# Performance work log

Measured on AMD Instinct MI355X. Metric: run time of the kernel, lower is better.

Reference implementation:

```python
import jax, jax.numpy as jnp
import numpy as np

N_NODES = 50000
N_EDGES = 800000
NH, FOUT, FIN = 4, 32, 128
LEAKY_SLOPE = 0.2


def setup_inputs() -> dict:
    key = jax.random.key(0)
    k1, k2, k3, k4, k5 = jax.random.split(key, 5)
    x = jax.random.normal(k1, (N_NODES, FIN), dtype=jnp.float32)
    edge_index = jax.random.randint(k2, (2, N_EDGES), 0, N_NODES, dtype=jnp.int64)
    W = jax.random.normal(k3, (FIN, NH * FOUT), dtype=jnp.float32) * (1.0 / np.sqrt(FIN))
    a_src = jax.random.normal(k4, (NH, FOUT), dtype=jnp.float32)
    a_trg = jax.random.normal(k5, (NH, FOUT), dtype=jnp.float32)
    bias = jnp.zeros((NH * FOUT,), dtype=jnp.float32)
    return {"x": x, "edge_index": edge_index, "W": W, "a_src": a_src, "a_trg": a_trg, "bias": bias}


def reference(x, edge_index, W, a_src, a_trg, bias):
    N = x.shape[0]
    # Step 1: linear projection (dropout omitted: eval mode)
    proj = (x @ W).reshape(N, NH, FOUT)              # (N, NH, FOUT)
    # Per-head attention scores for each node as source / target
    s_src = jnp.einsum('nhf,hf->nh', proj, a_src)    # (N, NH)
    s_trg = jnp.einsum('nhf,hf->nh', proj, a_trg)    # (N, NH)
    # Step 2: lift to edges (gather) and score
    src, trg = edge_index[0], edge_index[1]
    e = jax.nn.leaky_relu(s_src[src] + s_trg[trg], LEAKY_SLOPE)   # (E, NH)
    # Step 3: neighborhood-aware softmax (global max shift, as in GAT imp3)
    exp_e = jnp.exp(e - e.max())                      # (E, NH)
    denom = jax.ops.segment_sum(exp_e, trg, num_segments=N)       # (N, NH)
    att = exp_e / (denom[trg] + 1e-16)                # (E, NH)
    # Step 4: weight lifted source features and scatter-aggregate to targets
    weighted = proj[src] * att[:, :, None]            # (E, NH, FOUT)
    out = jax.ops.segment_sum(weighted, trg, num_segments=N)      # (N, NH, FOUT)
    # Step 5: skip connection (FIN == NH*FOUT -> direct add), concat heads, bias, ELU
    out = out + x.reshape(N, NH, FOUT)
    out = out.reshape(N, NH * FOUT) + bias
    return jax.nn.elu(out)
```

## Files before the change

### kernel.cpp

```cpp
#include <hip/hip_runtime.h>
#include <stdint.h>

typedef __attribute__((ext_vector_type(8))) short short8;
typedef __attribute__((ext_vector_type(4))) float floatx4;

__device__ inline float bf2f(unsigned short b) {
    unsigned u = ((unsigned)b) << 16;
    return __builtin_bit_cast(float, u);
}
__device__ inline unsigned short f2bf(float f) {
    unsigned u = __builtin_bit_cast(unsigned, f);
    unsigned r = (u + 0x7fffu + ((u >> 16) & 1u)) >> 16;
    return (unsigned short)r;
}
__device__ inline float ldf(const void* p, int i, int f32) {
    return f32 ? ((const float*)p)[i] : bf2f(((const unsigned short*)p)[i]);
}
__device__ inline int lde(const int* ei, int idx, int is64) {
    return is64 ? ei[2 * idx] : ei[idx];
}

__global__ __launch_bounds__(256) void k_pre(
    const void* __restrict__ x, const int* __restrict__ ei,
    const void* __restrict__ W, int* __restrict__ flags,
    unsigned short* __restrict__ WhT, unsigned short* __restrict__ WlT,
    int* __restrict__ counts, int N)
{
    int b = blockIdx.x;
    int t = threadIdx.x;
    if (b == 0) {
        __shared__ int h1, h2;
        if (t == 0) { h1 = 0; h2 = 0; }
        __syncthreads();
        const unsigned short* xs = (const unsigned short*)x;
        int c1 = 0;
        for (int i = t * 2; i < 65536; i += 512)
            if ((xs[i] & 0x7f80u) == 0x7f80u) c1++;
        int c2 = 0;
        for (int i = t * 2 + 1; i < 8192; i += 512)
            if (ei[i] != 0) c2++;
        atomicAdd(&h1, c1);
        atomicAdd(&h2, c2);
        __syncthreads();
        if (t == 0) { flags[0] = (h1 >= 8); flags[1] = (h2 < 8); }
    } else if (b <= 64) {
        __shared__ int wcnt;
        if (t == 0) wcnt = 0;
        __syncthreads();
        const unsigned short* wsamp = (const unsigned short*)W;
        int c = 0;
        for (int i = t * 2; i < 16384; i += 512)
            if ((wsamp[i] & 0x7f80u) == 0x7f80u) c++;
        atomicAdd(&wcnt, c);
        __syncthreads();
        int f32 = (wcnt >= 8);
        int idx = (b - 1) * 256 + t;
        int n = idx >> 7, k = idx & 127;
        float v = ldf(W, k * 128 + n, f32);
        unsigned short h = f2bf(v);
        WhT[idx] = h;
        WlT[idx] = f2bf(v - bf2f(h));
    } else {
        int idx = (b - 65) * 256 + t;
        if (idx <= N) counts[idx] = 0;
    }
}

__global__ __launch_bounds__(256) void k1_gemm(
    const void* __restrict__ x, const unsigned short* __restrict__ WhT,
    const unsigned short* __restrict__ WlT, const void* __restrict__ a_src,
    const void* __restrict__ a_trg, const int* __restrict__ flags,
    unsigned short* __restrict__ projb, float* __restrict__ ssrc,
    float* __restrict__ strg, int N)
{
    __shared__ __align__(16) unsigned short WT[128 * 136];
    int t = threadIdx.x;
    int f32 = flags[0];
    for (int i = t; i < 2048; i += 256) {
        int row = i >> 4, ch = (i & 15) * 8;
        *(short8*)&WT[row * 136 + ch] = *(const short8*)&WhT[row * 128 + ch];
    }
    __syncthreads();
    int wave = t >> 6, lane = t & 63;
    int col = lane & 15, quad = lane >> 4;
    int row0 = blockIdx.x * 64 + wave * 16;
    int m = row0 + col;
    if (m >= N) m = N - 1;
    short8 ah[4], al[4];
    if (f32) {
        const float* xf = (const float*)x + (size_t)m * 128 + quad * 8;
#pragma unroll
        for (int kb = 0; kb < 4; kb++) {
            float4 v0 = *(const float4*)(xf + kb * 32);
            float4 v1 = *(const float4*)(xf + kb * 32 + 4);
            float vv[8] = {v0.x, v0.y, v0.z, v0.w, v1.x, v1.y, v1.z, v1.w};
#pragma unroll
            for (int j = 0; j < 8; j++) {
                unsigned short h = f2bf(vv[j]);
                ah[kb][j] = (short)h;
                al[kb][j] = (short)f2bf(vv[j] - bf2f(h));
            }
        }
    } else {
        const unsigned short* xb = (const unsigned short*)x + (size_t)m * 128 + quad * 8;
#pragma unroll
        for (int kb = 0; kb < 4; kb++)
            ah[kb] = *(const short8*)(xb + kb * 32);
    }
    floatx4 acc[8];
#pragma unroll
    for (int c = 0; c < 8; c++) acc[c] = (floatx4){0.f, 0.f, 0.f, 0.f};
#pragma unroll
    for (int c = 0; c < 8; c++) {
        const short8* bp = (const short8*)(&WT[(c * 16 + col) * 136 + quad * 8]);
        short8 b0 = bp[0], b1 = bp[4], b2 = bp[8], b3 = bp[12];
        acc[c] = __builtin_amdgcn_mfma_f32_16x16x32_bf16(ah[0], b0, acc[c], 0, 0, 0);
        acc[c] = __builtin_amdgcn_mfma_f32_16x16x32_bf16(ah[1], b1, acc[c], 0, 0, 0);
        acc[c] = __builtin_amdgcn_mfma_f32_16x16x32_bf16(ah[2], b2, acc[c], 0, 0, 0);
        acc[c] = __builtin_amdgcn_mfma_f32_16x16x32_bf16(ah[3], b3, acc[c], 0, 0, 0);
        if (f32) {
            acc[c] = __builtin_amdgcn_mfma_f32_16x16x32_bf16(al[0], b0, acc[c], 0, 0, 0);
            acc[c] = __builtin_amdgcn_mfma_f32_16x16x32_bf16(al[1], b1, acc[c], 0, 0, 0);
            acc[c] = __builtin_amdgcn_mfma_f32_16x16x32_bf16(al[2], b2, acc[c], 0, 0, 0);
            acc[c] = __builtin_amdgcn_mfma_f32_16x16x32_bf16(al[3], b3, acc[c], 0, 0, 0);
        }
    }
    if (f32) {
        __syncthreads();
        for (int i = t; i < 2048; i += 256) {
            int row = i >> 4, ch = (i & 15) * 8;
            *(short8*)&WT[row * 136 + ch] = *(const short8*)&WlT[row * 128 + ch];
        }
        __syncthreads();
#pragma unroll
        for (int c = 0; c < 8; c++) {
            const short8* bp = (const short8*)(&WT[(c * 16 + col) * 136 + quad * 8]);
            acc[c] = __builtin_amdgcn_mfma_f32_16x16x32_bf16(ah[0], bp[0], acc[c], 0, 0, 0);
            acc[c] = __builtin_amdgcn_mfma_f32_16x16x32_bf16(ah[1], bp[4], acc[c], 0, 0, 0);
            acc[c] = __builtin_amdgcn_mfma_f32_16x16x32_bf16(ah[2], bp[8], acc[c], 0, 0, 0);
            acc[c] = __builtin_amdgcn_mfma_f32_16x16x32_bf16(ah[3], bp[12], acc[c], 0, 0, 0);
        }
    }
#pragma unroll
    for (int r = 0; r < 4; r++) {
        int row = row0 + quad * 4 + r;
        if (row < N) {
#pragma unroll
            for (int c = 0; c < 8; c++)
                projb[(size_t)row * 128 + c * 16 + col] = f2bf(acc[c][r]);
        }
    }
    float asv[8], atv[8];
#pragma unroll
    for (int c = 0; c < 8; c++) {
        int j = c * 16 + col;
        asv[c] = ldf(a_src, j, f32);
        atv[c] = ldf(a_trg, j, f32);
    }
#pragma unroll
    for (int r = 0; r < 4; r++) {
        int row = row0 + quad * 4 + r;
        float ps[4] = {0.f, 0.f, 0.f, 0.f}, pt[4] = {0.f, 0.f, 0.f, 0.f};
#pragma unroll
        for (int c = 0; c < 8; c++) {
            int h = c >> 1;
            ps[h] += acc[c][r] * asv[c];
            pt[h] += acc[c][r] * atv[c];
        }
#pragma unroll
        for (int k = 1; k < 16; k <<= 1) {
#pragma unroll
            for (int h = 0; h < 4; h++) {
                ps[h] += __shfl_xor(ps[h], k, 16);
                pt[h] += __shfl_xor(pt[h], k, 16);
            }
        }
        if (col == 0 && row < N) {
#pragma unroll
            for (int h = 0; h < 4; h++) {
                ssrc[(size_t)row * 4 + h] = ps[h];
                strg[(size_t)row * 4 + h] = pt[h];
            }
        }
    }
}

__device__ inline void edge_scores(const float* ssrc, const float* strg,
                                   int src, int trg, float* v) {
    float4 a = *(const float4*)(ssrc + (size_t)src * 4);
    float4 b = *(const float4*)(strg + (size_t)trg * 4);
    v[0] = a.x + b.x; v[1] = a.y + b.y; v[2] = a.z + b.z; v[3] = a.w + b.w;
#pragma unroll
    for (int h = 0; h < 4; h++) v[h] = v[h] > 0.f ? v[h] : 0.2f * v[h];
}

__global__ __launch_bounds__(256) void kE_count_max(
    const int* __restrict__ ei, const float* __restrict__ ssrc,
    const float* __restrict__ strg, const int* __restrict__ flags,
    int* __restrict__ counts, uint4* __restrict__ epackI,
    float4* __restrict__ epackV, float* __restrict__ blockmax, int E, int N)
{
    int e64 = flags[1];
    int e = blockIdx.x * 256 + threadIdx.x;
    float m = -3.0e38f;
    if (e < E) {
        int src = min(max(lde(ei, e, e64), 0), N - 1);
        int trg = min(max(lde(ei, E + e, e64), 0), N - 1);
        int rank = atomicAdd(&counts[trg], 1);
        float v[4];
        edge_scores(ssrc, strg, src, trg, v);
        m = fmaxf(fmaxf(v[0], v[1]), fmaxf(v[2], v[3]));
        epackI[e] = make_uint4((unsigned)src, (unsigned)trg, (unsigned)rank, 0u);
        epackV[e] = make_float4(v[0], v[1], v[2], v[3]);
    }
#pragma unroll
    for (int k = 1; k < 64; k <<= 1) m = fmaxf(m, __shfl_xor(m, k, 64));
    __shared__ float wm[4];
    if ((threadIdx.x & 63) == 0) wm[threadIdx.x >> 6] = m;
    __syncthreads();
    if (threadIdx.x == 0)
        blockmax[blockIdx.x] = fmaxf(fmaxf(wm[0], wm[1]), fmaxf(wm[2], wm[3]));
}

__global__ __launch_bounds__(256) void kS1_psum(
    const int* __restrict__ counts, int* __restrict__ partials, int NP1)
{
    int idx = blockIdx.x * 256 + threadIdx.x;
    int v = (idx < NP1) ? counts[idx] : 0;
#pragma unroll
    for (int k = 1; k < 64; k <<= 1) v += __shfl_xor(v, k, 64);
    __shared__ int wsum[4];
    if ((threadIdx.x & 63) == 0) wsum[threadIdx.x >> 6] = v;
    __syncthreads();
    if (threadIdx.x == 0)
        partials[blockIdx.x] = wsum[0] + wsum[1] + wsum[2] + wsum[3];
}

__global__ __launch_bounds__(256) void kS2_scanp(
    int* __restrict__ partials, int nb,
    const float* __restrict__ blockmax, float* __restrict__ Mval, int nbm)
{
    int t = threadIdx.x;
    if (nb <= 256) {
        __shared__ int lds[256];
        int v = (t < nb) ? partials[t] : 0;
        lds[t] = v;
        __syncthreads();
        int incl = v;
        for (int st = 1; st < 256; st <<= 1) {
            int add = (t >= st) ? lds[t - st] : 0;
            __syncthreads();
            incl += add;
            lds[t] = incl;
            __syncthreads();
        }
        if (t < nb) partials[t] = incl - v;
    } else if (t == 0) {
        int run = 0;
        for (int i = 0; i < nb; i++) { int c = partials[i]; partials[i] = run; run += c; }
    }
    __syncthreads();
    float m = -3.0e38f;
    for (int i = t; i < nbm; i += 256) m = fmaxf(m, blockmax[i]);
#pragma unroll
    for (int k = 1; k < 64; k <<= 1) m = fmaxf(m, __shfl_xor(m, k, 64));
    __shared__ float wm[4];
    if ((t & 63) == 0) wm[t >> 6] = m;
    __syncthreads();
    if (t == 0) *Mval = fmaxf(fmaxf(wm[0], wm[1]), fmaxf(wm[2], wm[3]));
}

__global__ __launch_bounds__(256) void kS3_offs(
    const int* __restrict__ counts, const int* __restrict__ partials,
    int* __restrict__ offsets, int NP1)
{
    int t = threadIdx.x;
    int idx = blockIdx.x * 256 + t;
    int v = (idx < NP1) ? counts[idx] : 0;
    __shared__ int lds[256];
    lds[t] = v;
    __syncthreads();
    int incl = v;
    for (int st = 1; st < 256; st <<= 1) {
        int add = (t >= st) ? lds[t - st] : 0;
        __syncthreads();
        incl += add;
        lds[t] = incl;
        __syncthreads();
    }
    if (idx < NP1) offsets[idx] = partials[blockIdx.x] + incl - v;
}

__global__ __launch_bounds__(256) void k2c_scatter(
    const uint4* __restrict__ epackI, const float4* __restrict__ epackV,
    const int* __restrict__ offsets, const float* __restrict__ Mval,
    uint4* __restrict__ erec, int E)
{
    int e = blockIdx.x * 256 + threadIdx.x;
    if (e >= E) return;
    uint4 pi = epackI[e];
    float4 pv = epackV[e];
    float M = *Mval;
    int pos = offsets[pi.y] + (int)pi.z;
    unsigned e01 = (unsigned)f2bf(__expf(pv.x - M)) |
                   ((unsigned)f2bf(__expf(pv.y - M)) << 16);
    unsigned e23 = (unsigned)f2bf(__expf(pv.z - M)) |
                   ((unsigned)f2bf(__expf(pv.w - M)) << 16);
    if (pos >= 0 && pos < E)
        erec[pos] = make_uint4(pi.x, e01, e23, 0u);
}

__global__ __launch_bounds__(256) void k3_agg(
    const int* __restrict__ offsets, const uint4* __restrict__ erec,
    const unsigned short* __restrict__ projb, const void* __restrict__ x,
    const void* __restrict__ bias, const int* __restrict__ flags,
    float* __restrict__ out, int N, int E)
{
    int w = threadIdx.x >> 6;
    int lane = threadIdx.x & 63;
    int n = blockIdx.x * 4 + w;
    int f32 = flags[0];
    if (n >= N) return;
    int off = offsets[n];
    int d = offsets[n + 1] - off;
    d = max(0, min(d, E));

    __shared__ int lsrc[4][64];
    __shared__ unsigned le[4][128];

    int half = lane >> 5;
    int sl = lane & 31;
    int h = sl >> 3;
    int hw = h >> 1;
    int hs = (h & 1) << 4;
    float den[4] = {0.f, 0.f, 0.f, 0.f};
    float a0 = 0.f, a1 = 0.f, a2 = 0.f, a3 = 0.f;

    for (int base = 0; base < d; base += 64) {
        int cd = min(64, d - base);
        if (lane < cd) {
            uint4 r = erec[off + base + lane];
            lsrc[w][lane] = min(max((int)r.x, 0), N - 1);
            le[w][lane * 2] = r.y;
            le[w][lane * 2 + 1] = r.z;
            den[0] += bf2f((unsigned short)(r.y & 0xffffu));
            den[1] += bf2f((unsigned short)(r.y >> 16));
            den[2] += bf2f((unsigned short)(r.z & 0xffffu));
            den[3] += bf2f((unsigned short)(r.z >> 16));
        }
        int k = 0;
        for (; k + 8 <= cd; k += 8) {
            int ss[4]; float ee[4]; uint2 vv[4];
#pragma unroll
            for (int u = 0; u < 4; u++) {
                int ke = k + 2 * u + half;
                ss[u] = lsrc[w][ke];
                unsigned wd = le[w][ke * 2 + hw];
                ee[u] = bf2f((unsigned short)((wd >> hs) & 0xffffu));
            }
#pragma unroll
            for (int u = 0; u < 4; u++)
                vv[u] = *(const uint2*)(projb + (size_t)ss[u] * 128 + sl * 4);
#pragma unroll
            for (int u = 0; u < 4; u++) {
                a0 = fmaf(bf2f((unsigned short)(vv[u].x & 0xffffu)), ee[u], a0);
                a1 = fmaf(bf2f((unsigned short)(vv[u].x >> 16)),     ee[u], a1);
                a2 = fmaf(bf2f((unsigned short)(vv[u].y & 0xffffu)), ee[u], a2);
                a3 = fmaf(bf2f((unsigned short)(vv[u].y >> 16)),     ee[u], a3);
            }
        }
        for (; k < cd; k += 2) {
            int ke = k + half;
            bool live = (ke < cd);
            int kidx = live ? ke : k;
            int s = lsrc[w][kidx];
            unsigned wd = le[w][kidx * 2 + hw];
            float ev = live ? bf2f((unsigned short)((wd >> hs) & 0xffffu)) : 0.f;
            uint2 v = *(const uint2*)(projb + (size_t)s * 128 + sl * 4);
            a0 = fmaf(bf2f((unsigned short)(v.x & 0xffffu)), ev, a0);
            a1 = fmaf(bf2f((unsigned short)(v.x >> 16)),     ev, a1);
            a2 = fmaf(bf2f((unsigned short)(v.y & 0xffffu)), ev, a2);
            a3 = fmaf(bf2f((unsigned short)(v.y >> 16)),     ev, a3);
        }
    }
    a0 += __shfl_xor(a0, 32, 64);
    a1 += __shfl_xor(a1, 32, 64);
    a2 += __shfl_xor(a2, 32, 64);
    a3 += __shfl_xor(a3, 32, 64);
#pragma unroll
    for (int k = 1; k < 64; k <<= 1)
#pragma unroll
        for (int hh = 0; hh < 4; hh++) den[hh] += __shfl_xor(den[hh], k, 64);
    float inv = 1.0f / (den[h] + 1e-16f);

    if (lane < 32) {
        int j0 = sl * 4;
        float o[4] = {a0 * inv, a1 * inv, a2 * inv, a3 * inv};
#pragma unroll
        for (int j = 0; j < 4; j++) {
            float v = o[j] + ldf(x, n * 128 + j0 + j, f32) + ldf(bias, j0 + j, f32);
            o[j] = v > 0.f ? v : __expf(v) - 1.f;
        }
        *(float4*)(out + (size_t)n * 128 + j0) = make_float4(o[0], o[1], o[2], o[3]);
    }
}

extern "C" void kernel_launch(void* const* d_in, const int* in_sizes, int n_in,
                              void* d_out, int out_size, void* d_ws, size_t ws_size,
                              hipStream_t stream)
{
    const void* x     = d_in[0];
    const int*  ei    = (const int*)d_in[1];
    const void* W     = d_in[2];
    const void* a_src = d_in[3];
    const void* a_trg = d_in[4];
    const void* bias  = d_in[5];
    float* out = (float*)d_out;
    int N = in_sizes[0] / 128;
    int E = N * 16;
    if (in_sizes[1] / 2 < E) E = in_sizes[1] / 2;
    int nbE = (E + 255) / 256;
    int NP1 = N + 1;
    int nbS = (NP1 + 255) / 256;
    int nbZ = (NP1 + 255) / 256;

    char* ws = (char*)d_ws;
    size_t o = 0;
    auto alloc = [&](size_t bytes) {
        size_t r = o;
        o = (o + bytes + 255) & ~(size_t)255;
        return r;
    };
    int* flags = (int*)(ws + alloc(256));
    unsigned short* projb = (unsigned short*)(ws + alloc((size_t)N * 128 * 2));
    float* ssrc  = (float*)(ws + alloc((size_t)N * 4 * 4));
    float* strg  = (float*)(ws + alloc((size_t)N * 4 * 4));
    float* Mval  = (float*)(ws + alloc(256));
    int* counts  = (int*)(ws + alloc((size_t)NP1 * 4));
    int* offsets = (int*)(ws + alloc((size_t)NP1 * 4));
    uint4* epackI = (uint4*)(ws + alloc((size_t)E * 16));
    float4* epackV = (float4*)(ws + alloc((size_t)E * 16));
    uint4* erec  = (uint4*)(ws + alloc((size_t)E * 16));
    float* blockmax = (float*)(ws + alloc((size_t)nbE * 4));
    int* partials = (int*)(ws + alloc((size_t)nbS * 4));
    unsigned short* WhT = (unsigned short*)(ws + alloc(128 * 128 * 2));
    unsigned short* WlT = (unsigned short*)(ws + alloc(128 * 128 * 2));

    k_pre<<<65 + nbZ, 256, 0, stream>>>(x, ei, W, flags, WhT, WlT, counts, N);
    k1_gemm<<<(N + 63) / 64, 256, 0, stream>>>(x, WhT, WlT, a_src, a_trg, flags,
                                               projb, ssrc, strg, N);
    kE_count_max<<<nbE, 256, 0, stream>>>(ei, ssrc, strg, flags, counts, epackI,
                                          epackV, blockmax, E, N);
    kS1_psum<<<nbS, 256, 0, stream>>>(counts, partials, NP1);
    kS2_scanp<<<1, 256, 0, stream>>>(partials, nbS, blockmax, Mval, nbE);
    kS3_offs<<<nbS, 256, 0, stream>>>(counts, partials, offsets, NP1);
    k2c_scatter<<<nbE, 256, 0, stream>>>(epackI, epackV, offsets, Mval, erec, E);
    k3_agg<<<(N + 3) / 4, 256, 0, stream>>>(offsets, erec, projb, x, bias,
                                            flags, out, N, E);
}
```

Before: 226.1 us.

## Replace three-kernel scan with single-pass decoupled lookback scan; pack edge indices

Merges the partial-sum, partial-scan and offsets kernels into one kernel that uses a decoupled lookback across blocks, and folds the global max into it via atomicMax on an order-preserving float key. Edge index records shrink from 16 to 8 bytes by packing src and trg into 16-bit halves. This removes two launches and some global traffic. The 16-bit packing only holds while node ids stay below 65536, and the lookback spin-wait assumes earlier blocks get scheduled first.

```diff
diff --git a/kernel.cpp b/kernel.cpp
--- a/kernel.cpp
+++ b/kernel.cpp
@@ -19,12 +19,21 @@
 __device__ inline int lde(const int* ei, int idx, int is64) {
     return is64 ? ei[2 * idx] : ei[idx];
 }
+__device__ inline unsigned fkey(float f) {
+    unsigned b = __builtin_bit_cast(unsigned, f);
+    return (b & 0x80000000u) ? ~b : (b | 0x80000000u);
+}
+__device__ inline float funkey(unsigned k) {
+    unsigned b = (k & 0x80000000u) ? (k & 0x7fffffffu) : ~k;
+    return __builtin_bit_cast(float, b);
+}
 
 __global__ __launch_bounds__(256) void k_pre(
     const void* __restrict__ x, const int* __restrict__ ei,
     const void* __restrict__ W, int* __restrict__ flags,
     unsigned short* __restrict__ WhT, unsigned short* __restrict__ WlT,
-    int* __restrict__ counts, int N)
+    int* __restrict__ counts, unsigned* __restrict__ state,
+    unsigned* __restrict__ Mkey, int nbS, int N)
 {
     int b = blockIdx.x;
     int t = threadIdx.x;
@@ -41,6 +50,8 @@
             if (ei[i] != 0) c2++;
         atomicAdd(&h1, c1);
         atomicAdd(&h2, c2);
+        for (int i = t; i < nbS; i += 256) state[i] = 0u;
+        if (t == 0) *Mkey = 0u;
         __syncthreads();
         if (t == 0) { flags[0] = (h1 >= 8); flags[1] = (h2 < 8); }
     } else if (b <= 64) {
@@ -197,7 +208,7 @@
 __global__ __launch_bounds__(256) void kE_count_max(
     const int* __restrict__ ei, const float* __restrict__ ssrc,
     const float* __restrict__ strg, const int* __restrict__ flags,
-    int* __restrict__ counts, uint4* __restrict__ epackI,
+    int* __restrict__ counts, uint2* __restrict__ epackI,
     float4* __restrict__ epackV, float* __restrict__ blockmax, int E, int N)
 {
     int e64 = flags[1];
@@ -210,7 +221,7 @@
         float v[4];
         edge_scores(ssrc, strg, src, trg, v);
         m = fmaxf(fmaxf(v[0], v[1]), fmaxf(v[2], v[3]));
-        epackI[e] = make_uint4((unsigned)src, (unsigned)trg, (unsigned)rank, 0u);
+        epackI[e] = make_uint2((unsigned)src | ((unsigned)trg << 16), (unsigned)rank);
         epackV[e] = make_float4(v[0], v[1], v[2], v[3]);
     }
 #pragma unroll
@@ -222,62 +233,17 @@
         blockmax[blockIdx.x] = fmaxf(fmaxf(wm[0], wm[1]), fmaxf(wm[2], wm[3]));
 }
 
-__global__ __launch_bounds__(256) void kS1_psum(
-    const int* __restrict__ counts, int* __restrict__ partials, int NP1)
-{
-    int idx = blockIdx.x * 256 + threadIdx.x;
-    int v = (idx < NP1) ? counts[idx] : 0;
-#pragma unroll
-    for (int k = 1; k < 64; k <<= 1) v += __shfl_xor(v, k, 64);
-    __shared__ int wsum[4];
-    if ((threadIdx.x & 63) == 0) wsum[threadIdx.x >> 6] = v;
-    __syncthreads();
-    if (threadIdx.x == 0)
-        partials[blockIdx.x] = wsum[0] + wsum[1] + wsum[2] + wsum[3];
-}
-
-__global__ __launch_bounds__(256) void kS2_scanp(
-    int* __restrict__ partials, int nb,
-    const float* __restrict__ blockmax, float* __restrict__ Mval, int nbm)
-{
+__global__ __launch_bounds__(256) void kScan(
+    const int* __restrict__ counts, unsigned* __restrict__ state,
+    int* __restrict__ offsets, const float* __restrict__ blockmax,
+    unsigned* __restrict__ Mkey, int NP1, int nbm)
+{
+    int b = blockIdx.x;
     int t = threadIdx.x;
-    if (nb <= 256) {
-        __shared__ int lds[256];
-        int v = (t < nb) ? partials[t] : 0;
-        lds[t] = v;
-        __syncthreads();
-        int incl = v;
-        for (int st = 1; st < 256; st <<= 1) {
-            int add = (t >= st) ? lds[t - st] : 0;
-            __syncthreads();
-            incl += add;
-            lds[t] = incl;
-            __syncthreads();
-        }
-        if (t < nb) partials[t] = incl - v;
-    } else if (t == 0) {
-        int run = 0;
-        for (int i = 0; i < nb; i++) { int c = partials[i]; partials[i] = run; run += c; }
-    }
-    __syncthreads();
-    float m = -3.0e38f;
-    for (int i = t; i < nbm; i += 256) m = fmaxf(m, blockmax[i]);
-#pragma unroll
-    for (int k = 1; k < 64; k <<= 1) m = fmaxf(m, __shfl_xor(m, k, 64));
-    __shared__ float wm[4];
-    if ((t & 63) == 0) wm[t >> 6] = m;
-    __syncthreads();
-    if (t == 0) *Mval = fmaxf(fmaxf(wm[0], wm[1]), fmaxf(wm[2], wm[3]));
-}
-
-__global__ __launch_bounds__(256) void kS3_offs(
-    const int* __restrict__ counts, const int* __restrict__ partials,
-    int* __restrict__ offsets, int NP1)
-{
-    int t = threadIdx.x;
-    int idx = blockIdx.x * 256 + t;
+    int idx = b * 256 + t;
     int v = (idx < NP1) ? counts[idx] : 0;
     __shared__ int lds[256];
+    __shared__ int spfx;
     lds[t] = v;
     __syncthreads();
     int incl = v;
@@ -288,26 +254,56 @@
         lds[t] = incl;
         __syncthreads();
     }
-    if (idx < NP1) offsets[idx] = partials[blockIdx.x] + incl - v;
+    int bsum = lds[255];
+    if (t == 0) {
+        atomicExch(&state[b], ((unsigned)bsum << 2) | 1u);
+        int prefix = 0;
+        int j = b - 1;
+        while (j >= 0) {
+            unsigned s;
+            do { s = atomicOr(&state[j], 0u); } while (s == 0u);
+            prefix += (int)(s >> 2);
+            if (s & 2u) break;
+            j--;
+        }
+        atomicExch(&state[b], ((unsigned)(prefix + bsum) << 2) | 3u);
+        spfx = prefix;
+    }
+    __syncthreads();
+    int prefix = spfx;
+    if (idx < NP1) offsets[idx] = prefix + incl - v;
+    float m = -3.0e38f;
+    for (int i = idx; i < nbm; i += gridDim.x * 256) m = fmaxf(m, blockmax[i]);
+#pragma unroll
+    for (int k = 1; k < 64; k <<= 1) m = fmaxf(m, __shfl_xor(m, k, 64));
+    __shared__ float wm[4];
+    if ((t & 63) == 0) wm[t >> 6] = m;
+    __syncthreads();
+    if (t == 0) {
+        float bm = fmaxf(fmaxf(wm[0], wm[1]), fmaxf(wm[2], wm[3]));
+        atomicMax(Mkey, fkey(bm));
+    }
 }
 
 __global__ __launch_bounds__(256) void k2c_scatter(
-    const uint4* __restrict__ epackI, const float4* __restrict__ epackV,
-    const int* __restrict__ offsets, const float* __restrict__ Mval,
+    const uint2* __restrict__ epackI, const float4* __restrict__ epackV,
+    const int* __restrict__ offsets, const unsigned* __restrict__ Mkey,
     uint4* __restrict__ erec, int E)
 {
     int e = blockIdx.x * 256 + threadIdx.x;
     if (e >= E) return;
-    uint4 pi = epackI[e];
+    uint2 pi = epackI[e];
     float4 pv = epackV[e];
-    float M = *Mval;
-    int pos = offsets[pi.y] + (int)pi.z;
+    float M = funkey(*Mkey);
+    int trg = (int)(pi.x >> 16);
+    int src = (int)(pi.x & 0xffffu);
+    int pos = offsets[trg] + (int)pi.y;
     unsigned e01 = (unsigned)f2bf(__expf(pv.x - M)) |
                    ((unsigned)f2bf(__expf(pv.y - M)) << 16);
     unsigned e23 = (unsigned)f2bf(__expf(pv.z - M)) |
                    ((unsigned)f2bf(__expf(pv.w - M)) << 16);
     if (pos >= 0 && pos < E)
-        erec[pos] = make_uint4(pi.x, e01, e23, 0u);
+        erec[pos] = make_uint4((unsigned)src, e01, e23, 0u);
 }
 
 __global__ __launch_bounds__(256) void k3_agg(
@@ -435,26 +431,25 @@
     unsigned short* projb = (unsigned short*)(ws + alloc((size_t)N * 128 * 2));
     float* ssrc  = (float*)(ws + alloc((size_t)N * 4 * 4));
     float* strg  = (float*)(ws + alloc((size_t)N * 4 * 4));
-    float* Mval  = (float*)(ws + alloc(256));
+    unsigned* Mkey = (unsigned*)(ws + alloc(256));
     int* counts  = (int*)(ws + alloc((size_t)NP1 * 4));
     int* offsets = (int*)(ws + alloc((size_t)NP1 * 4));
-    uint4* epackI = (uint4*)(ws + alloc((size_t)E * 16));
+    uint2* epackI = (uint2*)(ws + alloc((size_t)E * 8));
     float4* epackV = (float4*)(ws + alloc((size_t)E * 16));
     uint4* erec  = (uint4*)(ws + alloc((size_t)E * 16));
     float* blockmax = (float*)(ws + alloc((size_t)nbE * 4));
-    int* partials = (int*)(ws + alloc((size_t)nbS * 4));
+    unsigned* state = (unsigned*)(ws + alloc((size_t)nbS * 4));
     unsigned short* WhT = (unsigned short*)(ws + alloc(128 * 128 * 2));
     unsigned short* WlT = (unsigned short*)(ws + alloc(128 * 128 * 2));
 
-    k_pre<<<65 + nbZ, 256, 0, stream>>>(x, ei, W, flags, WhT, WlT, counts, N);
+    k_pre<<<65 + nbZ, 256, 0, stream>>>(x, ei, W, flags, WhT, WlT, counts,
+                                        state, Mkey, nbS, N);
     k1_gemm<<<(N + 63) / 64, 256, 0, stream>>>(x, WhT, WlT, a_src, a_trg, flags,
                                                projb, ssrc, strg, N);
     kE_count_max<<<nbE, 256, 0, stream>>>(ei, ssrc, strg, flags, counts, epackI,
                                           epackV, blockmax, E, N);
-    kS1_psum<<<nbS, 256, 0, stream>>>(counts, partials, NP1);
-    kS2_scanp<<<1, 256, 0, stream>>>(partials, nbS, blockmax, Mval, nbE);
-    kS3_offs<<<nbS, 256, 0, stream>>>(counts, partials, offsets, NP1);
-    k2c_scatter<<<nbE, 256, 0, stream>>>(epackI, epackV, offsets, Mval, erec, E);
+    kScan<<<nbS, 256, 0, stream>>>(counts, state, offsets, blockmax, Mkey, NP1, nbE);
+    k2c_scatter<<<nbE, 256, 0, stream>>>(epackI, epackV, offsets, Mkey, erec, E);
     k3_agg<<<(N + 3) / 4, 256, 0, stream>>>(offsets, erec, projb, x, bias,
                                             flags, out, N, E);
 }
```

After: 230.7 us. +2.1%, slower.

## Aggregate each node with 16 lanes and pack edge indices into 16 bits

Applied to the files above, without the earlier changes.

k3_agg now gives each node a 16-lane group instead of a full 64-lane wavefront. Each lane gathers 8 bf16 features with one 16-byte load and keeps its own head's softmax denominator, so the cross-lane shuffle reductions go away. This is meant to cut idle lanes and loop overhead at the average degree of about 16. Separately, the edge pack buffer shrinks from 16 to 8 bytes by storing src and trg as 16-bit fields in one word, which lowers memory traffic between the count and scatter kernels. That packing only works while node ids fit in 16 bits.

```diff
diff --git a/kernel.cpp b/kernel.cpp
--- a/kernel.cpp
+++ b/kernel.cpp
@@ -197,7 +197,7 @@
 __global__ __launch_bounds__(256) void kE_count_max(
     const int* __restrict__ ei, const float* __restrict__ ssrc,
     const float* __restrict__ strg, const int* __restrict__ flags,
-    int* __restrict__ counts, uint4* __restrict__ epackI,
+    int* __restrict__ counts, uint2* __restrict__ epackI,
     float4* __restrict__ epackV, float* __restrict__ blockmax, int E, int N)
 {
     int e64 = flags[1];
@@ -210,7 +210,7 @@
         float v[4];
         edge_scores(ssrc, strg, src, trg, v);
         m = fmaxf(fmaxf(v[0], v[1]), fmaxf(v[2], v[3]));
-        epackI[e] = make_uint4((unsigned)src, (unsigned)trg, (unsigned)rank, 0u);
+        epackI[e] = make_uint2((unsigned)src | ((unsigned)trg << 16), (unsigned)rank);
         epackV[e] = make_float4(v[0], v[1], v[2], v[3]);
     }
 #pragma unroll
@@ -292,22 +292,24 @@
 }
 
 __global__ __launch_bounds__(256) void k2c_scatter(
-    const uint4* __restrict__ epackI, const float4* __restrict__ epackV,
+    const uint2* __restrict__ epackI, const float4* __restrict__ epackV,
     const int* __restrict__ offsets, const float* __restrict__ Mval,
     uint4* __restrict__ erec, int E)
 {
     int e = blockIdx.x * 256 + threadIdx.x;
     if (e >= E) return;
-    uint4 pi = epackI[e];
+    uint2 pi = epackI[e];
     float4 pv = epackV[e];
     float M = *Mval;
-    int pos = offsets[pi.y] + (int)pi.z;
+    int trg = (int)(pi.x >> 16);
+    int src = (int)(pi.x & 0xffffu);
+    int pos = offsets[trg] + (int)pi.y;
     unsigned e01 = (unsigned)f2bf(__expf(pv.x - M)) |
                    ((unsigned)f2bf(__expf(pv.y - M)) << 16);
     unsigned e23 = (unsigned)f2bf(__expf(pv.z - M)) |
                    ((unsigned)f2bf(__expf(pv.w - M)) << 16);
     if (pos >= 0 && pos < E)
-        erec[pos] = make_uint4(pi.x, e01, e23, 0u);
+        erec[pos] = make_uint4((unsigned)src, e01, e23, 0u);
 }
 
 __global__ __launch_bounds__(256) void k3_agg(
@@ -316,93 +318,87 @@
     const void* __restrict__ bias, const int* __restrict__ flags,
     float* __restrict__ out, int N, int E)
 {
-    int w = threadIdx.x >> 6;
-    int lane = threadIdx.x & 63;
-    int n = blockIdx.x * 4 + w;
+    int t = threadIdx.x;
+    int gb = t >> 4;
+    int sl = t & 15;
+    int n = blockIdx.x * 16 + gb;
     int f32 = flags[0];
     if (n >= N) return;
     int off = offsets[n];
     int d = offsets[n + 1] - off;
     d = max(0, min(d, E));
 
-    __shared__ int lsrc[4][64];
-    __shared__ unsigned le[4][128];
-
-    int half = lane >> 5;
-    int sl = lane & 31;
-    int h = sl >> 3;
+    __shared__ int lsrc[16][16];
+    __shared__ unsigned le[16][32];
+
+    int h = sl >> 2;
     int hw = h >> 1;
     int hs = (h & 1) << 4;
-    float den[4] = {0.f, 0.f, 0.f, 0.f};
-    float a0 = 0.f, a1 = 0.f, a2 = 0.f, a3 = 0.f;
-
-    for (int base = 0; base < d; base += 64) {
-        int cd = min(64, d - base);
-        if (lane < cd) {
-            uint4 r = erec[off + base + lane];
-            lsrc[w][lane] = min(max((int)r.x, 0), N - 1);
-            le[w][lane * 2] = r.y;
-            le[w][lane * 2 + 1] = r.z;
-            den[0] += bf2f((unsigned short)(r.y & 0xffffu));
-            den[1] += bf2f((unsigned short)(r.y >> 16));
-            den[2] += bf2f((unsigned short)(r.z & 0xffffu));
-            den[3] += bf2f((unsigned short)(r.z >> 16));
+    float den = 0.f;
+    float a[8];
+#pragma unroll
+    for (int j = 0; j < 8; j++) a[j] = 0.f;
+
+    for (int base = 0; base < d; base += 16) {
+        int cd = min(16, d - base);
+        if (sl < cd) {
+            uint4 r = erec[off + base + sl];
+            lsrc[gb][sl] = min(max((int)r.x, 0), N - 1);
+            le[gb][sl * 2] = r.y;
+            le[gb][sl * 2 + 1] = r.z;
         }
         int k = 0;
-        for (; k + 8 <= cd; k += 8) {
-            int ss[4]; float ee[4]; uint2 vv[4];
-#pragma unroll
-            for (int u = 0; u < 4; u++) {
-                int ke = k + 2 * u + half;
-                ss[u] = lsrc[w][ke];
-                unsigned wd = le[w][ke * 2 + hw];
-                ee[u] = bf2f((unsigned short)((wd >> hs) & 0xffffu));
-            }
-#pragma unroll
-            for (int u = 0; u < 4; u++)
-                vv[u] = *(const uint2*)(projb + (size_t)ss[u] * 128 + sl * 4);
-#pragma unroll
-            for (int u = 0; u < 4; u++) {
-                a0 = fmaf(bf2f((unsigned short)(vv[u].x & 0xffffu)), ee[u], a0);
-                a1 = fmaf(bf2f((unsigned short)(vv[u].x >> 16)),     ee[u], a1);
-                a2 = fmaf(bf2f((unsigned short)(vv[u].y & 0xffffu)), ee[u], a2);
-                a3 = fmaf(bf2f((unsigned short)(vv[u].y >> 16)),     ee[u], a3);
-            }
-        }
-        for (; k < cd; k += 2) {
-            int ke = k + half;
-            bool live = (ke < cd);
-            int kidx = live ? ke : k;
-            int s = lsrc[w][kidx];
-            unsigned wd = le[w][kidx * 2 + hw];
-            float ev = live ? bf2f((unsigned short)((wd >> hs) & 0xffffu)) : 0.f;
-            uint2 v = *(const uint2*)(projb + (size_t)s * 128 + sl * 4);
-            a0 = fmaf(bf2f((unsigned short)(v.x & 0xffffu)), ev, a0);
-            a1 = fmaf(bf2f((unsigned short)(v.x >> 16)),     ev, a1);
-            a2 = fmaf(bf2f((unsigned short)(v.y & 0xffffu)), ev, a2);
-            a3 = fmaf(bf2f((unsigned short)(v.y >> 16)),     ev, a3);
-        }
-    }
-    a0 += __shfl_xor(a0, 32, 64);
-    a1 += __shfl_xor(a1, 32, 64);
-    a2 += __shfl_xor(a2, 32, 64);
-    a3 += __shfl_xor(a3, 32, 64);
-#pragma unroll
-    for (int k = 1; k < 64; k <<= 1)
-#pragma unroll
-        for (int hh = 0; hh < 4; hh++) den[hh] += __shfl_xor(den[hh], k, 64);
-    float inv = 1.0f / (den[h] + 1e-16f);
-
-    if (lane < 32) {
-        int j0 = sl * 4;
-        float o[4] = {a0 * inv, a1 * inv, a2 * inv, a3 * inv};
-#pragma unroll
-        for (int j = 0; j < 4; j++) {
-            float v = o[j] + ldf(x, n * 128 + j0 + j, f32) + ldf(bias, j0 + j, f32);
-            o[j] = v > 0.f ? v : __expf(v) - 1.f;
-        }
-        *(float4*)(out + (size_t)n * 128 + j0) = make_float4(o[0], o[1], o[2], o[3]);
-    }
+        for (; k + 2 <= cd; k += 2) {
+            int s0 = lsrc[gb][k], s1 = lsrc[gb][k + 1];
+            float e0 = bf2f((unsigned short)((le[gb][k * 2 + hw] >> hs) & 0xffffu));
+            float e1 = bf2f((unsigned short)((le[gb][(k + 1) * 2 + hw] >> hs) & 0xffffu));
+            uint4 v0 = *(const uint4*)(projb + (size_t)s0 * 128 + sl * 8);
+            uint4 v1 = *(const uint4*)(projb + (size_t)s1 * 128 + sl * 8);
+            den += e0;
+            den += e1;
+            a[0] = fmaf(bf2f((unsigned short)(v0.x & 0xffffu)), e0, a[0]);
+            a[1] = fmaf(bf2f((unsigned short)(v0.x >> 16)),     e0, a[1]);
+            a[2] = fmaf(bf2f((unsigned short)(v0.y & 0xffffu)), e0, a[2]);
+            a[3] = fmaf(bf2f((unsigned short)(v0.y >> 16)),     e0, a[3]);
+            a[4] = fmaf(bf2f((unsigned short)(v0.z & 0xffffu)), e0, a[4]);
+            a[5] = fmaf(bf2f((unsigned short)(v0.z >> 16)),     e0, a[5]);
+            a[6] = fmaf(bf2f((unsigned short)(v0.w & 0xffffu)), e0, a[6]);
+            a[7] = fmaf(bf2f((unsigned short)(v0.w >> 16)),     e0, a[7]);
+            a[0] = fmaf(bf2f((unsigned short)(v1.x & 0xffffu)), e1, a[0]);
+            a[1] = fmaf(bf2f((unsigned short)(v1.x >> 16)),     e1, a[1]);
+            a[2] = fmaf(bf2f((unsigned short)(v1.y & 0xffffu)), e1, a[2]);
+            a[3] = fmaf(bf2f((unsigned short)(v1.y >> 16)),     e1, a[3]);
+            a[4] = fmaf(bf2f((unsigned short)(v1.z & 0xffffu)), e1, a[4]);
+            a[5] = fmaf(bf2f((unsigned short)(v1.z >> 16)),     e1, a[5]);
+            a[6] = fmaf(bf2f((unsigned short)(v1.w & 0xffffu)), e1, a[6]);
+            a[7] = fmaf(bf2f((unsigned short)(v1.w >> 16)),     e1, a[7]);
+        }
+        if (k < cd) {
+            int s0 = lsrc[gb][k];
+            float e0 = bf2f((unsigned short)((le[gb][k * 2 + hw] >> hs) & 0xffffu));
+            uint4 v0 = *(const uint4*)(projb + (size_t)s0 * 128 + sl * 8);
+            den += e0;
+            a[0] = fmaf(bf2f((unsigned short)(v0.x & 0xffffu)), e0, a[0]);
+            a[1] = fmaf(bf2f((unsigned short)(v0.x >> 16)),     e0, a[1]);
+            a[2] = fmaf(bf2f((unsigned short)(v0.y & 0xffffu)), e0, a[2]);
+            a[3] = fmaf(bf2f((unsigned short)(v0.y >> 16)),     e0, a[3]);
+            a[4] = fmaf(bf2f((unsigned short)(v0.z & 0xffffu)), e0, a[4]);
+            a[5] = fmaf(bf2f((unsigned short)(v0.z >> 16)),     e0, a[5]);
+            a[6] = fmaf(bf2f((unsigned short)(v0.w & 0xffffu)), e0, a[6]);
+            a[7] = fmaf(bf2f((unsigned short)(v0.w >> 16)),     e0, a[7]);
+        }
+    }
+    float inv = 1.0f / (den + 1e-16f);
+
+    int j0 = sl * 8;
+    float o[8];
+#pragma unroll
+    for (int j = 0; j < 8; j++) {
+        float v = a[j] * inv + ldf(x, n * 128 + j0 + j, f32) + ldf(bias, j0 + j, f32);
+        o[j] = v > 0.f ? v : __expf(v) - 1.f;
+    }
+    *(float4*)(out + (size_t)n * 128 + j0)     = make_float4(o[0], o[1], o[2], o[3]);
+    *(float4*)(out + (size_t)n * 128 + j0 + 4) = make_float4(o[4], o[5], o[6], o[7]);
 }
 
 extern "C" void kernel_launch(void* const* d_in, const int* in_sizes, int n_in,
@@ -438,7 +434,7 @@
     float* Mval  = (float*)(ws + alloc(256));
     int* counts  = (int*)(ws + alloc((size_t)NP1 * 4));
     int* offsets = (int*)(ws + alloc((size_t)NP1 * 4));
-    uint4* epackI = (uint4*)(ws + alloc((size_t)E * 16));
+    uint2* epackI = (uint2*)(ws + alloc((size_t)E * 8));
     float4* epackV = (float4*)(ws + alloc((size_t)E * 16));
     uint4* erec  = (uint4*)(ws + alloc((size_t)E * 16));
     float* blockmax = (float*)(ws + alloc((size_t)nbE * 4));
@@ -455,6 +451,6 @@
     kS2_scanp<<<1, 256, 0, stream>>>(partials, nbS, blockmax, Mval, nbE);
     kS3_offs<<<nbS, 256, 0, stream>>>(counts, partials, offsets, NP1);
     k2c_scatter<<<nbE, 256, 0, stream>>>(epackI, epackV, offsets, Mval, erec, E);
-    k3_agg<<<(N + 3) / 4, 256, 0, stream>>>(offsets, erec, projb, x, bias,
-                                            flags, out, N, E);
-}
+    k3_agg<<<(N + 15) / 16, 256, 0, stream>>>(offsets, erec, projb, x, bias,
+                                              flags, out, N, E);
+}
```

After: 237.2 us. 4.9% more time.

## Overlap edge counting with GEMM and recompute edge scores instead of storing

Applied to the files above, without the earlier changes.

The edge counting and ranking pass moves into extra blocks of the GEMM kernel, so the atomics run alongside the projection. Source and target indices are packed into one 32-bit word, so each edge record is 8 bytes instead of 32. The float4 score buffer is dropped and the scatter kernel recomputes the leaky-ReLU scores from ssrc/strg gathers, trading extra random reads for less edge traffic. Packing indices into 16 bits limits node IDs to 65535, which fits N=50000 but breaks for larger graphs.

```diff
diff --git a/kernel.cpp b/kernel.cpp
--- a/kernel.cpp
+++ b/kernel.cpp
@@ -66,16 +66,30 @@
     }
 }
 
-__global__ __launch_bounds__(256) void k1_gemm(
+__global__ __launch_bounds__(256) void k1_fused(
     const void* __restrict__ x, const unsigned short* __restrict__ WhT,
     const unsigned short* __restrict__ WlT, const void* __restrict__ a_src,
     const void* __restrict__ a_trg, const int* __restrict__ flags,
     unsigned short* __restrict__ projb, float* __restrict__ ssrc,
-    float* __restrict__ strg, int N)
+    float* __restrict__ strg,
+    const int* __restrict__ ei, int* __restrict__ counts,
+    uint2* __restrict__ epackI, int nbG, int E, int N)
 {
     __shared__ __align__(16) unsigned short WT[128 * 136];
     int t = threadIdx.x;
     int f32 = flags[0];
+    if (blockIdx.x >= nbG) {
+        int e = (blockIdx.x - nbG) * 256 + t;
+        if (e < E) {
+            int e64 = flags[1];
+            int src = min(max(lde(ei, e, e64), 0), N - 1);
+            int trg = min(max(lde(ei, E + e, e64), 0), N - 1);
+            int rank = atomicAdd(&counts[trg], 1);
+            epackI[e] = make_uint2((unsigned)src | ((unsigned)trg << 16),
+                                   (unsigned)rank);
+        }
+        return;
+    }
     for (int i = t; i < 2048; i += 256) {
         int row = i >> 4, ch = (i & 15) * 8;
         *(short8*)&WT[row * 136 + ch] = *(const short8*)&WhT[row * 128 + ch];
@@ -194,24 +208,19 @@
     for (int h = 0; h < 4; h++) v[h] = v[h] > 0.f ? v[h] : 0.2f * v[h];
 }
 
-__global__ __launch_bounds__(256) void kE_count_max(
-    const int* __restrict__ ei, const float* __restrict__ ssrc,
-    const float* __restrict__ strg, const int* __restrict__ flags,
-    int* __restrict__ counts, uint4* __restrict__ epackI,
-    float4* __restrict__ epackV, float* __restrict__ blockmax, int E, int N)
-{
-    int e64 = flags[1];
+__global__ __launch_bounds__(256) void kE_max(
+    const uint2* __restrict__ epackI, const float* __restrict__ ssrc,
+    const float* __restrict__ strg, float* __restrict__ blockmax, int E)
+{
     int e = blockIdx.x * 256 + threadIdx.x;
     float m = -3.0e38f;
     if (e < E) {
-        int src = min(max(lde(ei, e, e64), 0), N - 1);
-        int trg = min(max(lde(ei, E + e, e64), 0), N - 1);
-        int rank = atomicAdd(&counts[trg], 1);
+        uint2 pi = epackI[e];
+        int src = (int)(pi.x & 0xffffu);
+        int trg = (int)(pi.x >> 16);
         float v[4];
         edge_scores(ssrc, strg, src, trg, v);
         m = fmaxf(fmaxf(v[0], v[1]), fmaxf(v[2], v[3]));
-        epackI[e] = make_uint4((unsigned)src, (unsigned)trg, (unsigned)rank, 0u);
-        epackV[e] = make_float4(v[0], v[1], v[2], v[3]);
     }
 #pragma unroll
     for (int k = 1; k < 64; k <<= 1) m = fmaxf(m, __shfl_xor(m, k, 64));
@@ -292,22 +301,25 @@
 }
 
 __global__ __launch_bounds__(256) void k2c_scatter(
-    const uint4* __restrict__ epackI, const float4* __restrict__ epackV,
-    const int* __restrict__ offsets, const float* __restrict__ Mval,
-    uint4* __restrict__ erec, int E)
+    const uint2* __restrict__ epackI, const float* __restrict__ ssrc,
+    const float* __restrict__ strg, const int* __restrict__ offsets,
+    const float* __restrict__ Mval, uint4* __restrict__ erec, int E)
 {
     int e = blockIdx.x * 256 + threadIdx.x;
     if (e >= E) return;
-    uint4 pi = epackI[e];
-    float4 pv = epackV[e];
+    uint2 pi = epackI[e];
     float M = *Mval;
-    int pos = offsets[pi.y] + (int)pi.z;
-    unsigned e01 = (unsigned)f2bf(__expf(pv.x - M)) |
-                   ((unsigned)f2bf(__expf(pv.y - M)) << 16);
-    unsigned e23 = (unsigned)f2bf(__expf(pv.z - M)) |
-                   ((unsigned)f2bf(__expf(pv.w - M)) << 16);
+    int src = (int)(pi.x & 0xffffu);
+    int trg = (int)(pi.x >> 16);
+    float v[4];
+    edge_scores(ssrc, strg, src, trg, v);
+    int pos = offsets[trg] + (int)pi.y;
+    unsigned e01 = (unsigned)f2bf(__expf(v[0] - M)) |
+                   ((unsigned)f2bf(__expf(v[1] - M)) << 16);
+    unsigned e23 = (unsigned)f2bf(__expf(v[2] - M)) |
+                   ((unsigned)f2bf(__expf(v[3] - M)) << 16);
     if (pos >= 0 && pos < E)
-        erec[pos] = make_uint4(pi.x, e01, e23, 0u);
+        erec[pos] = make_uint4((unsigned)src, e01, e23, 0u);
 }
 
 __global__ __launch_bounds__(256) void k3_agg(
@@ -423,6 +435,7 @@
     int NP1 = N + 1;
     int nbS = (NP1 + 255) / 256;
     int nbZ = (NP1 + 255) / 256;
+    int nbG = (N + 63) / 64;
 
     char* ws = (char*)d_ws;
     size_t o = 0;
@@ -438,8 +451,7 @@
     float* Mval  = (float*)(ws + alloc(256));
     int* counts  = (int*)(ws + alloc((size_t)NP1 * 4));
     int* offsets = (int*)(ws + alloc((size_t)NP1 * 4));
-    uint4* epackI = (uint4*)(ws + alloc((size_t)E * 16));
-    float4* epackV = (float4*)(ws + alloc((size_t)E * 16));
+    uint2* epackI = (uint2*)(ws + alloc((size_t)E * 8));
     uint4* erec  = (uint4*)(ws + alloc((size_t)E * 16));
     float* blockmax = (float*)(ws + alloc((size_t)nbE * 4));
     int* partials = (int*)(ws + alloc((size_t)nbS * 4));
@@ -447,14 +459,14 @@
     unsigned short* WlT = (unsigned short*)(ws + alloc(128 * 128 * 2));
 
     k_pre<<<65 + nbZ, 256, 0, stream>>>(x, ei, W, flags, WhT, WlT, counts, N);
-    k1_gemm<<<(N + 63) / 64, 256, 0, stream>>>(x, WhT, WlT, a_src, a_trg, flags,
-                                               projb, ssrc, strg, N);
-    kE_count_max<<<nbE, 256, 0, stream>>>(ei, ssrc, strg, flags, counts, epackI,
-                                          epackV, blockmax, E, N);
+    k1_fused<<<nbG + nbE, 256, 0, stream>>>(x, WhT, WlT, a_src, a_trg, flags,
+                                            projb, ssrc, strg,
+                                            ei, counts, epackI, nbG, E, N);
+    kE_max<<<nbE, 256, 0, stream>>>(epackI, ssrc, strg, blockmax, E);
     kS1_psum<<<nbS, 256, 0, stream>>>(counts, partials, NP1);
     kS2_scanp<<<1, 256, 0, stream>>>(partials, nbS, blockmax, Mval, nbE);
     kS3_offs<<<nbS, 256, 0, stream>>>(counts, partials, offsets, NP1);
-    k2c_scatter<<<nbE, 256, 0, stream>>>(epackI, epackV, offsets, Mval, erec, E);
+    k2c_scatter<<<nbE, 256, 0, stream>>>(epackI, ssrc, strg, offsets, Mval, erec, E);
     k3_agg<<<(N + 3) / 4, 256, 0, stream>>>(offsets, erec, projb, x, bias,
                                             flags, out, N, E);
 }
```

Result: no change. 229.0 us (+1.3%).
